# Kernel optimization log

Measured on AMD Instinct MI355X. Metric: run time of the kernel, lower is better.

The kernel has to match this reference:

```python
import jax, jax.numpy as jnp
import numpy as np

D_MODEL = 1024
HEAD_DIM = 64

def setup_inputs() -> dict:
    key = jax.random.key(0)
    ks = jax.random.split(key, 7)
    x = jax.random.normal(ks[0], (4, 4096, D_MODEL), dtype=jnp.float32)
    s = 1.0 / np.sqrt(D_MODEL)
    Wq = jax.random.uniform(ks[1], (D_MODEL, HEAD_DIM), jnp.float32, -s, s)
    bq = jax.random.uniform(ks[2], (HEAD_DIM,), jnp.float32, -s, s)
    Wk = jax.random.uniform(ks[3], (D_MODEL, HEAD_DIM), jnp.float32, -s, s)
    bk = jax.random.uniform(ks[4], (HEAD_DIM,), jnp.float32, -s, s)
    Wv = jax.random.uniform(ks[5], (D_MODEL, HEAD_DIM), jnp.float32, -s, s)
    bv = jax.random.uniform(ks[6], (HEAD_DIM,), jnp.float32, -s, s)
    return {"x": x, "Wq": Wq, "bq": bq, "Wk": Wk, "bk": bk, "Wv": Wv, "bv": bv}

def reference(x, Wq, bq, Wk, bk, Wv, bv):
    B, T, _ = x.shape
    q = x @ Wq + bq  # [B, T, H]
    k = x @ Wk + bk
    v = x @ Wv + bv
    scale = 1.0 / jnp.sqrt(jnp.asarray(q.shape[-1], q.dtype))
    scores = jnp.einsum('bqh,bkh->bqk', q, k) * scale  # [B, T, T]
    causal = jnp.tril(jnp.ones((T, T), dtype=bool))
    scores = jnp.where(causal, scores, jnp.asarray(-jnp.inf, scores.dtype))
    attn = jax.nn.softmax(scores, axis=-1)
    return jnp.einsum('bqk,bkh->bqh', attn, v)
```

## Files before the change

kernel.cpp:

```cpp
#include <hip/hip_runtime.h>

#define BATCH 4
#define SEQ 4096
#define DMODEL 1024
#define HDIM 64

#define QBLK 64
#define NQT 64
#define CHUNK 256
#define ITERS 8
#define BSLOT 544
#define MAXC 17

#define QSCALE 0.18033688f

typedef _Float16 h16;
typedef _Float16 h16x8 __attribute__((ext_vector_type(8)));
typedef _Float16 h16x4 __attribute__((ext_vector_type(4)));
typedef float f32x4 __attribute__((ext_vector_type(4)));
typedef float f32x16 __attribute__((ext_vector_type(16)));

#define WF_ELEMS (12 * 32 * 64 * 8)
#define QK_ELEMS (BATCH * SEQ * HDIM)
#define PB 262144
#define NSLOT (BATCH * BSLOT)

__device__ __forceinline__ int slot_base(int qt) {
    int a = qt >> 2, b = qt & 3;
    return (a + 1) * (2 * a + b);
}

__device__ __forceinline__ int kperm(int u) {
    return (u & 3) | (((u >> 2) & 1) << 3) | (((u >> 3) & 1) << 2);
}

template<int OFF>
__device__ __forceinline__ void gload_o(h16x8& dst, const h16* p) {
    asm volatile("global_load_dwordx4 %0, %1, off offset:%2" : "=v"(dst) : "v"(p), "n"(OFF));
}

__global__ __launch_bounds__(256) void prep(const float* __restrict__ Wq,
                                            const float* __restrict__ Wk,
                                            const float* __restrict__ Wv,
                                            const float* __restrict__ x,
                                            h16* __restrict__ Wf,
                                            h16* __restrict__ xh) {
    int b = blockIdx.x;
    if (b < 96) {
        int flat = b * 256 + threadIdx.x;
        int lane = flat & 63;
        int kt = (flat >> 6) & 31;
        int fg = flat >> 11;
        int col = 16 * fg + (lane & 15);
        const float* W = (col < 64) ? Wq : (col < 128) ? Wk : Wv;
        int c = col & 63;
        int k0 = 32 * kt + 8 * (lane >> 4);
        h16x8 v;
        #pragma unroll
        for (int j = 0; j < 8; j++) v[j] = (h16)W[(size_t)(k0 + j) * 64 + c];
        *(h16x8*)(Wf + (size_t)flat * 8) = v;
        return;
    }
    size_t flat = (size_t)(b - 96) * 256 + threadIdx.x;
    int lane = (int)(flat & 63);
    int kt = (int)((flat >> 6) & 31);
    int mt = (int)(flat >> 11);
    const float* xp = x + (size_t)(16 * mt + (lane & 15)) * DMODEL + 32 * kt + 8 * (lane >> 4);
    f32x4 lo = *(const f32x4*)xp;
    f32x4 hi = *(const f32x4*)(xp + 4);
    h16x8 v;
    #pragma unroll
    for (int j = 0; j < 4; j++) { v[j] = (h16)lo[j]; v[j + 4] = (h16)hi[j]; }
    *(h16x8*)(xh + flat * 8) = v;
}

#define QISSUE(S, IMM)                                                        \
    gload_o<IMM>(a##S##0, ax0); gload_o<IMM>(a##S##1, ax1);                   \
    gload_o<IMM>(b##S##0, w0);  gload_o<IMM>(b##S##1, w1);                    \
    gload_o<IMM>(b##S##2, w2);

#define QCOMPUTE(S)                                                           \
    c00 = __builtin_amdgcn_mfma_f32_16x16x32_f16(a##S##0, b##S##0, c00, 0, 0, 0); \
    c01 = __builtin_amdgcn_mfma_f32_16x16x32_f16(a##S##0, b##S##1, c01, 0, 0, 0); \
    c02 = __builtin_amdgcn_mfma_f32_16x16x32_f16(a##S##0, b##S##2, c02, 0, 0, 0); \
    c10 = __builtin_amdgcn_mfma_f32_16x16x32_f16(a##S##1, b##S##0, c10, 0, 0, 0); \
    c11 = __builtin_amdgcn_mfma_f32_16x16x32_f16(a##S##1, b##S##1, c11, 0, 0, 0); \
    c12 = __builtin_amdgcn_mfma_f32_16x16x32_f16(a##S##1, b##S##2, c12, 0, 0, 0);

#define QSTEP(S, N) {                                                         \
    asm volatile("s_waitcnt vmcnt(" #N ")" ::: "memory");                     \
    __builtin_amdgcn_sched_barrier(0);                                        \
    QCOMPUTE(S)                                                               \
    QISSUE(S, 3072)                                                           \
    ax0 += 512; ax1 += 512; w0 += 512; w1 += 512; w2 += 512; }

#define QSTEP_T(S, N) {                                                       \
    asm volatile("s_waitcnt vmcnt(" #N ")" ::: "memory");                     \
    __builtin_amdgcn_sched_barrier(0);                                        \
    QCOMPUTE(S) }

__global__ __launch_bounds__(256, 2) void qkv_proj(
    const h16* __restrict__ xh, const h16* __restrict__ Wf,
    const float* __restrict__ bq, const float* __restrict__ bk, const float* __restrict__ bv,
    h16* __restrict__ Qf, h16* __restrict__ Kf, h16* __restrict__ Vf)
{
    int lane = threadIdx.x & 63;
    int w = threadIdx.x >> 6;
    int r0 = blockIdx.x * 32;
    int ln15 = lane & 15;

    const h16* ax0 = xh + (size_t)(2 * blockIdx.x) * 16384 + lane * 8 + 512;
    const h16* ax1 = ax0 + 16384;
    const h16* w0 = Wf + (size_t)(3 * w) * 16384 + lane * 8 + 512;
    const h16* w1 = w0 + 16384;
    const h16* w2 = w0 + 32768;

    h16x8 aA0, aA1, bA0, bA1, bA2;
    h16x8 aB0, aB1, bB0, bB1, bB2;
    h16x8 aC0, aC1, bC0, bC1, bC2;
    h16x8 aD0, aD1, bD0, bD1, bD2;
    f32x4 c00 = {}, c01 = {}, c02 = {}, c10 = {}, c11 = {}, c12 = {};

    QISSUE(A, -1024) QISSUE(B, 0) QISSUE(C, 1024) QISSUE(D, 2048)

    QSTEP(A, 15) QSTEP(B, 15) QSTEP(C, 15) QSTEP(D, 15)
    QSTEP(A, 15) QSTEP(B, 15) QSTEP(C, 15) QSTEP(D, 15)
    QSTEP(A, 15) QSTEP(B, 15) QSTEP(C, 15) QSTEP(D, 15)
    QSTEP(A, 15) QSTEP(B, 15) QSTEP(C, 15) QSTEP(D, 15)
    QSTEP(A, 15) QSTEP(B, 15) QSTEP(C, 15) QSTEP(D, 15)
    QSTEP(A, 15) QSTEP(B, 15) QSTEP(C, 15) QSTEP(D, 15)
    QSTEP(A, 15) QSTEP(B, 15) QSTEP(C, 15) QSTEP(D, 15)
    QSTEP_T(A, 15) QSTEP_T(B, 10) QSTEP_T(C, 5) QSTEP_T(D, 0)

    f32x4 acc[2][3] = {{c00, c01, c02}, {c10, c11, c12}};
    #pragma unroll
    for (int f = 0; f < 3; f++) {
        int col = 48 * w + 16 * f + ln15;
        float bias = (col < 64) ? bq[col] : (col < 128) ? bk[col - 64] : bv[col - 128];
        #pragma unroll
        for (int m = 0; m < 2; m++) {
            #pragma unroll
            for (int i = 0; i < 4; i++) {
                int t = r0 + 16 * m + (lane >> 4) * 4 + i;
                int bb = t >> 12;
                int tt = t & (SEQ - 1);
                float v = acc[m][f][i] + bias;
                if (col < 64) {
                    int d = col >> 4, hh = (col >> 3) & 1, e = col & 7;
                    Qf[(size_t)bb * PB + (tt >> 5) * 2048 + d * 512 +
                       (hh * 32 + (tt & 31)) * 8 + e] = (h16)(v * QSCALE);
                } else if (col < 128) {
                    int ck = col - 64;
                    int d = ck >> 4, hh = (ck >> 3) & 1, e = ck & 7;
                    Kf[(size_t)bb * PB + (tt >> 5) * 2048 + d * 512 +
                       (hh * 32 + (tt & 31)) * 8 + e] = (h16)v;
                } else {
                    int h = col - 128;
                    int tp = (tt & ~15) | kperm(tt & 15);
                    int j = ((h >> 5) << 1) | ((tp >> 4) & 1);
                    Vf[(size_t)bb * PB + (tp >> 5) * 2048 + j * 512 +
                       (((tp >> 3) & 1) * 32 + (h & 31)) * 8 + (tp & 7)] = (h16)v;
                }
            }
        }
    }
}

__device__ __forceinline__ void flash_compute(
    h16x8 K0, h16x8 K1, h16x8 K2, h16x8 K3,
    h16x8 V0, h16x8 V1, h16x8 V2, h16x8 V3,
    h16x8 q0v, h16x8 q1v, h16x8 q2v, h16x8 q3v,
    int kt0, int q0g, int qg, int hi,
    f32x16& o0, f32x16& o1, float& m_i, float& l_i)
{
    f32x16 s = {};
    s = __builtin_amdgcn_mfma_f32_32x32x16_f16(K0, q0v, s, 0, 0, 0);
    s = __builtin_amdgcn_mfma_f32_32x32x16_f16(K1, q1v, s, 0, 0, 0);
    s = __builtin_amdgcn_mfma_f32_32x32x16_f16(K2, q2v, s, 0, 0, 0);
    s = __builtin_amdgcn_mfma_f32_32x32x16_f16(K3, q3v, s, 0, 0, 0);

    float sc[16];
    #pragma unroll
    for (int r = 0; r < 16; r++) sc[r] = s[r];
    if (kt0 + 31 > q0g) {
        #pragma unroll
        for (int r = 0; r < 16; r++) {
            int kg = kt0 + (r & 3) + 8 * (r >> 2) + 4 * hi;
            if (kg > qg) sc[r] = -1e30f;
        }
    }
    float tm = sc[0];
    #pragma unroll
    for (int r = 1; r < 16; r++) tm = fmaxf(tm, sc[r]);
    tm = fmaxf(tm, __shfl_xor(tm, 32));

    if (!__all(tm - m_i <= 8.f)) {
        float mn = fmaxf(m_i, tm);
        float al = exp2f(m_i - mn);
        m_i = mn;
        l_i *= al;
        #pragma unroll
        for (int r = 0; r < 16; r++) { o0[r] *= al; o1[r] *= al; }
    }

    float p[16], rs = 0.f;
    #pragma unroll
    for (int r = 0; r < 16; r++) { p[r] = exp2f(sc[r] - m_i); rs += p[r]; }
    rs += __shfl_xor(rs, 32);
    l_i += rs;

    h16x8 pb0, pb1;
    #pragma unroll
    for (int j = 0; j < 8; j++) { pb0[j] = (h16)p[j]; pb1[j] = (h16)p[8 + j]; }

    o0 = __builtin_amdgcn_mfma_f32_32x32x16_f16(V0, pb0, o0, 0, 0, 0);
    o0 = __builtin_amdgcn_mfma_f32_32x32x16_f16(V1, pb1, o0, 0, 0, 0);
    o1 = __builtin_amdgcn_mfma_f32_32x32x16_f16(V2, pb0, o1, 0, 0, 0);
    o1 = __builtin_amdgcn_mfma_f32_32x32x16_f16(V3, pb1, o1, 0, 0, 0);
}

#define ISSUE(B) {                                                            \
    gload_o<0>(k##B##0, kp);    gload_o<1024>(k##B##1, kp);                   \
    gload_o<2048>(k##B##2, kp); gload_o<3072>(k##B##3, kp);                   \
    gload_o<0>(v##B##0, vp);    gload_o<1024>(v##B##1, vp);                   \
    gload_o<2048>(v##B##2, vp); gload_o<3072>(v##B##3, vp);                   \
    kp += 2048; vp += 2048; }

#define COMPUTE(B, T) {                                                       \
    __builtin_amdgcn_s_setprio(1);                                            \
    flash_compute(k##B##0, k##B##1, k##B##2, k##B##3,                         \
                  v##B##0, v##B##1, v##B##2, v##B##3,                         \
                  qa0, qa1, qa2, qa3, S + 32 * (T), q0, qg0, hi,              \
                  o00, o01, m0, l0);                                          \
    flash_compute(k##B##0, k##B##1, k##B##2, k##B##3,                         \
                  v##B##0, v##B##1, v##B##2, v##B##3,                         \
                  qc0, qc1, qc2, qc3, S + 32 * (T), q0 + 32, qg1, hi,         \
                  o10, o11, m1, l1);                                          \
    __builtin_amdgcn_s_setprio(0); }

#define STEP(CUR, NXT, T) {                                                   \
    ISSUE(NXT)                                                                \
    asm volatile("s_waitcnt vmcnt(8)" ::: "memory");                          \
    __builtin_amdgcn_sched_barrier(0);                                        \
    COMPUTE(CUR, T) }

#define STEP_LAST(CUR, T) {                                                   \
    asm volatile("s_waitcnt vmcnt(0)" ::: "memory");                          \
    __builtin_amdgcn_sched_barrier(0);                                        \
    COMPUTE(CUR, T) }

__global__ __launch_bounds__(256, 2) void flash(
    const h16* __restrict__ Qf, const h16* __restrict__ Kf, const h16* __restrict__ Vf,
    h16* __restrict__ o_part, float* __restrict__ ml_part)
{
    int wid = threadIdx.x >> 6;
    int lane = threadIdx.x & 63;
    int bid = blockIdx.x;
    int batch = bid / 136;
    int s = bid - batch * 136;
    int a = (int)((sqrtf(8.f * s + 1.f) - 1.f) * 0.5f);
    while ((a + 1) * (a + 2) / 2 <= s) a++;
    while (a * (a + 1) / 2 > s) a--;
    int c = s - a * (a + 1) / 2;
    int qt = 4 * a + wid;

    int q0 = qt * QBLK;
    int S = c * CHUNK;
    int l31 = lane & 31;
    int hi = lane >> 5;
    int qg0 = q0 + l31;
    int qg1 = q0 + 32 + l31;

    const h16* kp = Kf + (size_t)batch * PB + (S >> 5) * 2048 + lane * 8;
    const h16* vp = Vf + (size_t)batch * PB + (S >> 5) * 2048 + lane * 8;

    h16x8 qa0, qa1, qa2, qa3, qc0, qc1, qc2, qc3;
    {
        const h16* qp = Qf + (size_t)batch * PB + (q0 >> 5) * 2048 + lane * 8;
        gload_o<0>(qa0, qp); gload_o<1024>(qa1, qp);
        gload_o<2048>(qa2, qp); gload_o<3072>(qa3, qp);
        const h16* qp2 = qp + 2048;
        gload_o<0>(qc0, qp2); gload_o<1024>(qc1, qp2);
        gload_o<2048>(qc2, qp2); gload_o<3072>(qc3, qp2);
    }

    h16x8 kA0, kA1, kA2, kA3, vA0, vA1, vA2, vA3;
    h16x8 kB0, kB1, kB2, kB3, vB0, vB1, vB2, vB3;

    f32x16 o00 = {}, o01 = {}, o10 = {}, o11 = {};
    float m0 = -1e30f, l0 = 0.f, m1 = -1e30f, l1 = 0.f;

    ISSUE(A)

    STEP(A, B, 0)
    STEP(B, A, 1)
    STEP(A, B, 2)
    STEP(B, A, 3)
    STEP(A, B, 4)
    STEP(B, A, 5)
    STEP(A, B, 6)
    STEP_LAST(B, 7)

    size_t slot = (size_t)batch * BSLOT + slot_base(qt) + c;
    h16* opb = o_part + slot * (QBLK * 64);
    {
        float inv = 1.f / l0;
        h16* op = opb + l31 * 64;
        #pragma unroll
        for (int q = 0; q < 4; q++) {
            h16x4 pk0, pk1;
            #pragma unroll
            for (int i = 0; i < 4; i++) {
                pk0[i] = (h16)(o00[4 * q + i] * inv);
                pk1[i] = (h16)(o01[4 * q + i] * inv);
            }
            *(h16x4*)(op + 8 * q + 4 * hi) = pk0;
            *(h16x4*)(op + 32 + 8 * q + 4 * hi) = pk1;
        }
    }
    {
        float inv = 1.f / l1;
        h16* op = opb + (32 + l31) * 64;
        #pragma unroll
        for (int q = 0; q < 4; q++) {
            h16x4 pk0, pk1;
            #pragma unroll
            for (int i = 0; i < 4; i++) {
                pk0[i] = (h16)(o10[4 * q + i] * inv);
                pk1[i] = (h16)(o11[4 * q + i] * inv);
            }
            *(h16x4*)(op + 8 * q + 4 * hi) = pk0;
            *(h16x4*)(op + 32 + 8 * q + 4 * hi) = pk1;
        }
    }
    if (hi == 0) {
        ml_part[slot * 128 + l31 * 2] = m0;
        ml_part[slot * 128 + l31 * 2 + 1] = l0;
        ml_part[slot * 128 + (32 + l31) * 2] = m1;
        ml_part[slot * 128 + (32 + l31) * 2 + 1] = l1;
    }
}

__global__ __launch_bounds__(256) void combine(
    const h16* __restrict__ o_part, const float* __restrict__ ml_part,
    float* __restrict__ out)
{
    __shared__ float mlds[MAXC * 128];
    int bid = blockIdx.x;
    int rq = bid & 3;
    int tile = bid >> 2;
    int batch = tile >> 6;
    int qt = tile & (NQT - 1);
    int q0 = qt * QBLK;
    int nc = (qt >> 2) + 1;
    size_t base = (size_t)batch * BSLOT + slot_base(qt);

    for (int i = threadIdx.x; i < nc * 128; i += 256)
        mlds[i] = ml_part[base * 128 + i];
    __syncthreads();

    int r = rq * 16 + (threadIdx.x >> 4);
    int c4 = (threadIdx.x & 15) * 4;

    float M = -1e30f;
    for (int c = 0; c < nc; c++) M = fmaxf(M, mlds[c * 128 + r * 2]);

    const h16* op = o_part + base * (QBLK * 64) + r * 64 + c4;
    float L = 0.f;
    f32x4 A = {};
    #pragma unroll 4
    for (int c = 0; c < nc; c++) {
        float wt = exp2f(mlds[c * 128 + r * 2] - M) * mlds[c * 128 + r * 2 + 1];
        L += wt;
        h16x4 v = *(const h16x4*)(op + (size_t)c * (QBLK * 64));
        A[0] += wt * (float)v[0];
        A[1] += wt * (float)v[1];
        A[2] += wt * (float)v[2];
        A[3] += wt * (float)v[3];
    }
    f32x4 o;
    float inv = 1.f / L;
    #pragma unroll
    for (int j = 0; j < 4; j++) o[j] = A[j] * inv;
    *(f32x4*)(out + ((size_t)batch * SEQ + q0 + r) * HDIM + c4) = o;
}

extern "C" void kernel_launch(void* const* d_in, const int* in_sizes, int n_in,
                              void* d_out, int out_size, void* d_ws, size_t ws_size,
                              hipStream_t stream) {
    const float* x  = (const float*)d_in[0];
    const float* Wq = (const float*)d_in[1];
    const float* bq = (const float*)d_in[2];
    const float* Wk = (const float*)d_in[3];
    const float* bk = (const float*)d_in[4];
    const float* Wv = (const float*)d_in[5];
    const float* bv = (const float*)d_in[6];
    float* out = (float*)d_out;

    h16* Wf = (h16*)d_ws;
    h16* Qf = Wf + WF_ELEMS;
    h16* Kf = Qf + QK_ELEMS;
    h16* Vf = Kf + QK_ELEMS;
    h16* xh = Vf + QK_ELEMS;
    h16* o_part = xh;
    float* ml_part = (float*)(o_part + (size_t)NSLOT * QBLK * 64);

    hipLaunchKernelGGL(prep, dim3(96 + 8192), dim3(256), 0, stream, Wq, Wk, Wv, x, Wf, xh);
    hipLaunchKernelGGL(qkv_proj, dim3(512), dim3(256), 0, stream,
                       xh, Wf, bq, bk, bv, Qf, Kf, Vf);
    hipLaunchKernelGGL(flash, dim3(BATCH * 136), dim3(256), 0, stream,
                       Qf, Kf, Vf, o_part, ml_part);
    hipLaunchKernelGGL(combine, dim3(BATCH * NQT * 4), dim3(256), 0, stream,
                       o_part, ml_part, out);
}
```

Measured before the change: 71.76 us.

## Fuse fp32-to-fp16 conversion of x into QKV projection via LDS double buffering

```diff
diff --git a/kernel.cpp b/kernel.cpp
--- a/kernel.cpp
+++ b/kernel.cpp
@@ -38,99 +38,101 @@
 __device__ __forceinline__ void gload_o(h16x8& dst, const h16* p) {
     asm volatile("global_load_dwordx4 %0, %1, off offset:%2" : "=v"(dst) : "v"(p), "n"(OFF));
 }
-
-__global__ __launch_bounds__(256) void prep(const float* __restrict__ Wq,
-                                            const float* __restrict__ Wk,
-                                            const float* __restrict__ Wv,
-                                            const float* __restrict__ x,
-                                            h16* __restrict__ Wf,
-                                            h16* __restrict__ xh) {
-    int b = blockIdx.x;
-    if (b < 96) {
-        int flat = b * 256 + threadIdx.x;
-        int lane = flat & 63;
-        int kt = (flat >> 6) & 31;
-        int fg = flat >> 11;
-        int col = 16 * fg + (lane & 15);
-        const float* W = (col < 64) ? Wq : (col < 128) ? Wk : Wv;
-        int c = col & 63;
-        int k0 = 32 * kt + 8 * (lane >> 4);
-        h16x8 v;
-        #pragma unroll
-        for (int j = 0; j < 8; j++) v[j] = (h16)W[(size_t)(k0 + j) * 64 + c];
-        *(h16x8*)(Wf + (size_t)flat * 8) = v;
-        return;
-    }
-    size_t flat = (size_t)(b - 96) * 256 + threadIdx.x;
-    int lane = (int)(flat & 63);
-    int kt = (int)((flat >> 6) & 31);
-    int mt = (int)(flat >> 11);
-    const float* xp = x + (size_t)(16 * mt + (lane & 15)) * DMODEL + 32 * kt + 8 * (lane >> 4);
-    f32x4 lo = *(const f32x4*)xp;
-    f32x4 hi = *(const f32x4*)(xp + 4);
+template<int OFF>
+__device__ __forceinline__ void gloadf_o(f32x4& dst, const float* p) {
+    asm volatile("global_load_dwordx4 %0, %1, off offset:%2" : "=v"(dst) : "v"(p), "n"(OFF));
+}
+
+#define MFMA16(a, b, c) __builtin_amdgcn_mfma_f32_16x16x32_f16(a, b, c, 0, 0, 0)
+
+__global__ __launch_bounds__(256) void prep_w(const float* __restrict__ Wq,
+                                              const float* __restrict__ Wk,
+                                              const float* __restrict__ Wv,
+                                              h16* __restrict__ Wf) {
+    int flat = blockIdx.x * 256 + threadIdx.x;
+    int lane = flat & 63;
+    int kt = (flat >> 6) & 31;
+    int fg = flat >> 11;
+    int col = 16 * fg + (lane & 15);
+    const float* W = (col < 64) ? Wq : (col < 128) ? Wk : Wv;
+    int c = col & 63;
+    int k0 = 32 * kt + 8 * (lane >> 4);
     h16x8 v;
     #pragma unroll
-    for (int j = 0; j < 4; j++) { v[j] = (h16)lo[j]; v[j + 4] = (h16)hi[j]; }
-    *(h16x8*)(xh + flat * 8) = v;
-}
-
-#define QISSUE(S, IMM)                                                        \
-    gload_o<IMM>(a##S##0, ax0); gload_o<IMM>(a##S##1, ax1);                   \
-    gload_o<IMM>(b##S##0, w0);  gload_o<IMM>(b##S##1, w1);                    \
-    gload_o<IMM>(b##S##2, w2);
-
-#define QCOMPUTE(S)                                                           \
-    c00 = __builtin_amdgcn_mfma_f32_16x16x32_f16(a##S##0, b##S##0, c00, 0, 0, 0); \
-    c01 = __builtin_amdgcn_mfma_f32_16x16x32_f16(a##S##0, b##S##1, c01, 0, 0, 0); \
-    c02 = __builtin_amdgcn_mfma_f32_16x16x32_f16(a##S##0, b##S##2, c02, 0, 0, 0); \
-    c10 = __builtin_amdgcn_mfma_f32_16x16x32_f16(a##S##1, b##S##0, c10, 0, 0, 0); \
-    c11 = __builtin_amdgcn_mfma_f32_16x16x32_f16(a##S##1, b##S##1, c11, 0, 0, 0); \
-    c12 = __builtin_amdgcn_mfma_f32_16x16x32_f16(a##S##1, b##S##2, c12, 0, 0, 0);
-
-#define QSTEP(S, N) {                                                         \
-    asm volatile("s_waitcnt vmcnt(" #N ")" ::: "memory");                     \
-    __builtin_amdgcn_sched_barrier(0);                                        \
-    QCOMPUTE(S)                                                               \
-    QISSUE(S, 3072)                                                           \
-    ax0 += 512; ax1 += 512; w0 += 512; w1 += 512; w2 += 512; }
-
-#define QSTEP_T(S, N) {                                                       \
-    asm volatile("s_waitcnt vmcnt(" #N ")" ::: "memory");                     \
-    __builtin_amdgcn_sched_barrier(0);                                        \
-    QCOMPUTE(S) }
-
-__global__ __launch_bounds__(256, 2) void qkv_proj(
-    const h16* __restrict__ xh, const h16* __restrict__ Wf,
+    for (int j = 0; j < 8; j++) v[j] = (h16)W[(size_t)(k0 + j) * 64 + c];
+    *(h16x8*)(Wf + (size_t)flat * 8) = v;
+}
+
+#define XISSUE(R, S) { gloadf_o<(S) * 256>(R##a, xp); gloadf_o<(S) * 256 + 16>(R##b, xp); }
+
+#define WISSUE(S) {                                                           \
+    gload_o<0>(wr##S##0, w0); gload_o<1024>(wr##S##1, w0);                    \
+    gload_o<0>(wr##S##2, w1); gload_o<1024>(wr##S##3, w1);                    \
+    gload_o<0>(wr##S##4, w2); gload_o<1024>(wr##S##5, w2);                    \
+    w0 += 1024; w1 += 1024; w2 += 1024; }
+
+#define XWRITE(R, P) {                                                        \
+    h16x8 v_;                                                                 \
+    _Pragma("unroll")                                                         \
+    for (int j_ = 0; j_ < 4; j_++) { v_[j_] = (h16)R##a[j_]; v_[4 + j_] = (h16)R##b[j_]; } \
+    *(h16x8*)(&xbuf[P][wo]) = v_; }
+
+#define QCOMP(S, P) {                                                         \
+    h16x8 a00 = *(const h16x8*)(&xbuf[P][lane * 8]);                          \
+    h16x8 a01 = *(const h16x8*)(&xbuf[P][512 + lane * 8]);                    \
+    c00 = MFMA16(a00, wr##S##0, c00); c01 = MFMA16(a00, wr##S##2, c01);       \
+    c02 = MFMA16(a00, wr##S##4, c02);                                         \
+    c10 = MFMA16(a01, wr##S##0, c10); c11 = MFMA16(a01, wr##S##2, c11);       \
+    c12 = MFMA16(a01, wr##S##4, c12);                                         \
+    h16x8 a10 = *(const h16x8*)(&xbuf[P][1024 + lane * 8]);                   \
+    h16x8 a11 = *(const h16x8*)(&xbuf[P][1536 + lane * 8]);                   \
+    c00 = MFMA16(a10, wr##S##1, c00); c01 = MFMA16(a10, wr##S##3, c01);       \
+    c02 = MFMA16(a10, wr##S##5, c02);                                         \
+    c10 = MFMA16(a11, wr##S##1, c10); c11 = MFMA16(a11, wr##S##3, c11);       \
+    c12 = MFMA16(a11, wr##S##5, c12); }
+
+#define VM0 { asm volatile("s_waitcnt vmcnt(0)" ::: "memory");                \
+              __builtin_amdgcn_sched_barrier(0); }
+
+#define STGE(s) { QCOMP(A, 0) VM0 XWRITE(xB, 1) XISSUE(xA, (s) + 2) WISSUE(A) __syncthreads(); }
+#define STGO(s) { QCOMP(B, 1) VM0 XWRITE(xA, 0) XISSUE(xB, (s) + 2) WISSUE(B) __syncthreads(); }
+
+__global__ __launch_bounds__(256, 2) void qkv_fused(
+    const float* __restrict__ x, const h16* __restrict__ Wf,
     const float* __restrict__ bq, const float* __restrict__ bk, const float* __restrict__ bv,
     h16* __restrict__ Qf, h16* __restrict__ Kf, h16* __restrict__ Vf)
 {
-    int lane = threadIdx.x & 63;
-    int w = threadIdx.x >> 6;
+    __shared__ h16 xbuf[2][2048];
+    int t = threadIdx.x;
+    int lane = t & 63;
+    int w = t >> 6;
     int r0 = blockIdx.x * 32;
     int ln15 = lane & 15;
 
-    const h16* ax0 = xh + (size_t)(2 * blockIdx.x) * 16384 + lane * 8 + 512;
-    const h16* ax1 = ax0 + 16384;
-    const h16* w0 = Wf + (size_t)(3 * w) * 16384 + lane * 8 + 512;
+    const float* xp = x + (size_t)(r0 + (t >> 3)) * DMODEL + (t & 7) * 8;
+    int wo = ((t & 7) >> 2) * 1024 + ((t >> 3) >> 4) * 512 +
+             ((t & 3) * 16 + ((t >> 3) & 15)) * 8;
+    const h16* w0 = Wf + (size_t)(3 * w) * 16384 + lane * 8;
     const h16* w1 = w0 + 16384;
     const h16* w2 = w0 + 32768;
 
-    h16x8 aA0, aA1, bA0, bA1, bA2;
-    h16x8 aB0, aB1, bB0, bB1, bB2;
-    h16x8 aC0, aC1, bC0, bC1, bC2;
-    h16x8 aD0, aD1, bD0, bD1, bD2;
+    f32x4 xAa, xAb, xBa, xBb;
+    h16x8 wrA0, wrA1, wrA2, wrA3, wrA4, wrA5;
+    h16x8 wrB0, wrB1, wrB2, wrB3, wrB4, wrB5;
     f32x4 c00 = {}, c01 = {}, c02 = {}, c10 = {}, c11 = {}, c12 = {};
 
-    QISSUE(A, -1024) QISSUE(B, 0) QISSUE(C, 1024) QISSUE(D, 2048)
-
-    QSTEP(A, 15) QSTEP(B, 15) QSTEP(C, 15) QSTEP(D, 15)
-    QSTEP(A, 15) QSTEP(B, 15) QSTEP(C, 15) QSTEP(D, 15)
-    QSTEP(A, 15) QSTEP(B, 15) QSTEP(C, 15) QSTEP(D, 15)
-    QSTEP(A, 15) QSTEP(B, 15) QSTEP(C, 15) QSTEP(D, 15)
-    QSTEP(A, 15) QSTEP(B, 15) QSTEP(C, 15) QSTEP(D, 15)
-    QSTEP(A, 15) QSTEP(B, 15) QSTEP(C, 15) QSTEP(D, 15)
-    QSTEP(A, 15) QSTEP(B, 15) QSTEP(C, 15) QSTEP(D, 15)
-    QSTEP_T(A, 15) QSTEP_T(B, 10) QSTEP_T(C, 5) QSTEP_T(D, 0)
+    XISSUE(xA, 0) WISSUE(A) XISSUE(xB, 1) WISSUE(B)
+    asm volatile("s_waitcnt vmcnt(8)" ::: "memory");
+    __builtin_amdgcn_sched_barrier(0);
+    XWRITE(xA, 0)
+    __syncthreads();
+
+    STGE(0)  STGO(1)  STGE(2)  STGO(3)
+    STGE(4)  STGO(5)  STGE(6)  STGO(7)
+    STGE(8)  STGO(9)  STGE(10) STGO(11)
+    STGE(12) STGO(13)
+    { QCOMP(A, 0) VM0 XWRITE(xB, 1) __syncthreads(); }
+    { QCOMP(B, 1) }
 
     f32x4 acc[2][3] = {{c00, c01, c02}, {c10, c11, c12}};
     #pragma unroll
@@ -141,9 +143,9 @@
         for (int m = 0; m < 2; m++) {
             #pragma unroll
             for (int i = 0; i < 4; i++) {
-                int t = r0 + 16 * m + (lane >> 4) * 4 + i;
-                int bb = t >> 12;
-                int tt = t & (SEQ - 1);
+                int tr = r0 + 16 * m + (lane >> 4) * 4 + i;
+                int bb = tr >> 12;
+                int tt = tr & (SEQ - 1);
                 float v = acc[m][f][i] + bias;
                 if (col < 64) {
                     int d = col >> 4, hh = (col >> 3) & 1, e = col & 7;
@@ -401,13 +403,12 @@
     h16* Qf = Wf + WF_ELEMS;
     h16* Kf = Qf + QK_ELEMS;
     h16* Vf = Kf + QK_ELEMS;
-    h16* xh = Vf + QK_ELEMS;
-    h16* o_part = xh;
+    h16* o_part = Vf + QK_ELEMS;
     float* ml_part = (float*)(o_part + (size_t)NSLOT * QBLK * 64);
 
-    hipLaunchKernelGGL(prep, dim3(96 + 8192), dim3(256), 0, stream, Wq, Wk, Wv, x, Wf, xh);
-    hipLaunchKernelGGL(qkv_proj, dim3(512), dim3(256), 0, stream,
-                       xh, Wf, bq, bk, bv, Qf, Kf, Vf);
+    hipLaunchKernelGGL(prep_w, dim3(96), dim3(256), 0, stream, Wq, Wk, Wv, Wf);
+    hipLaunchKernelGGL(qkv_fused, dim3(512), dim3(256), 0, stream,
+                       x, Wf, bq, bk, bv, Qf, Kf, Vf);
     hipLaunchKernelGGL(flash, dim3(BATCH * 136), dim3(256), 0, stream,
                        Qf, Kf, Vf, o_part, ml_part);
     hipLaunchKernelGGL(combine, dim3(BATCH * NQT * 4), dim3(256), 0, stream,
```

New measurement: 62.32 us, median of 3. 1.15x faster.
